# Performance work log

Measured on AMD Instinct MI355X. Metric: run time of the kernel, lower is better.

The kernel has to match this reference:

```python
import jax, jax.numpy as jnp
import numpy as np

D, L, W, K = 16, 1000000, 64, 8
PAD = (W - 1) // 2  # 31, matches padding1 in the torch code


def setup_inputs() -> dict:
    key = jax.random.key(0)
    kx, kp = jax.random.split(key)
    x = jax.random.normal(kx, (D, L), dtype=jnp.float32)
    # torch uses torch.rand (uniform [0,1)) for each of the K (D,W) parameters
    P = jax.random.uniform(kp, (K, D, W), dtype=jnp.float32)
    return {"x": x, "P": P}


def _fullscan(x, P):
    # x: (D, L); P: (K, D, W)
    p = PAD
    # --- middle positions k in [p, L-W+p]: standard valid correlation ---
    # mid[k_out, o] = sum_{d,m} x[d, o+m] * P[k_out, d, m], position k = o + p
    mid = jax.lax.conv_general_dilated(
        x[None],                      # (1, D, L)
        P,                            # (K, D, W)
        window_strides=(1,),
        padding="VALID",
        dimension_numbers=("NCH", "OIH", "NCH"),
    )[0]                              # (K, L-W+1)
    # --- left edge k in [0, p): data x[:, :k+W-p] * kernel[:, :k+W-p] ---
    # prefix[i, m] = sum_d x[d, m] * P[i, d, m] over the first W samples
    tl = jnp.einsum("dm,kdm->km", x[:, :W], P)        # (K, W)
    left_c = jnp.cumsum(tl, axis=1)                    # prefix sums
    left = left_c[:, W - p - 1 : W - 1]                # (K, p)
    # --- right edge k in (L-W+p, L): data x[:, k-p:] * kernel[:, W+k-L-p:] ---
    tr = jnp.einsum("dm,kdm->km", x[:, L - W :], P)    # (K, W)
    suf = jnp.cumsum(tr[:, ::-1], axis=1)[:, ::-1]     # suffix sums: suf[:, t] = sum_{m>=t}
    right = suf[:, 1 : W - p]                          # (K, W-1-p)
    y = jnp.concatenate([left, mid, right], axis=1)    # (K, L)
    return y.reshape(-1, 1)                            # (K*L, 1)


def reference(x, P):
    return _fullscan(x, P)
```

## Files before the change

### kernel.cpp

```cpp
#include <hip/hip_runtime.h>


constexpr int D    = 16;
constexpr int L    = 1000000;
constexpr int W    = 64;
constexpr int K    = 8;
constexpr int PADL = 31;
constexpr int NMID = L - W + 1;
constexpr int TPB  = 256;
constexpr int OTW  = 8;
constexpr int CTW  = OTW + 2;
constexpr int BLK_OUT = 4 * OTW * 32;
constexpr int XS   = 1104;
constexpr int NBLK = (NMID + BLK_OUT - 1) / BLK_OUT;
constexpr int NGRID = NBLK + K;

typedef __attribute__((ext_vector_type(8)))  short short8;
typedef __attribute__((ext_vector_type(16))) float floatx16;

__device__ __forceinline__ unsigned short f2bf(float f) {
    union { float f; unsigned u; } v; v.f = f;
    unsigned u = v.u + 0x7fff + ((v.u >> 16) & 1);
    return (unsigned short)(u >> 16);
}

__global__ __launch_bounds__(TPB, 3) void fullscan_mid(
    const float* __restrict__ x, const float* __restrict__ P,
    const unsigned short* __restrict__ afr, float* __restrict__ out)
{
    __shared__ __align__(16) unsigned short xs[XS * 16];
    const int bid = blockIdx.x;
    const int tid = threadIdx.x;

    if (bid >= NBLK) {
        const int k = bid - NBLK;
        const int j = tid;
        if (j < PADL) {
            float acc = 0.0f;
            for (int m = 0; m <= 32 + j; ++m)
#pragma unroll
                for (int d = 0; d < D; ++d)
                    acc = fmaf(x[d * L + m], P[(k * D + d) * W + m], acc);
            out[k * L + j] = acc;
        } else if (j < 2 * PADL + 1) {
            const int jj = j - PADL;
            float acc = 0.0f;
            for (int m = jj + 1; m < W; ++m)
#pragma unroll
                for (int d = 0; d < D; ++d)
                    acc = fmaf(x[d * L + (L - W) + m], P[(k * D + d) * W + m], acc);
            out[k * L + PADL + NMID + jj] = acc;
        }
        return;
    }

    const int s0   = bid * BLK_OUT;
    const int lane = tid & 63;
    const int wv   = tid >> 6;

    short8 A[16];
#pragma unroll
    for (int c = 0; c < 16; ++c)
        A[c] = *(const short8*)(afr + (c * 64 + lane) * 8);

    {
        const int pl = tid & 63;
        const int dq = tid >> 6;
        const float* xr0 = x + (4 * dq + 0) * L + s0;
        const float* xr1 = x + (4 * dq + 1) * L + s0;
        const float* xr2 = x + (4 * dq + 2) * L + s0;
        const float* xr3 = x + (4 * dq + 3) * L + s0;
#pragma unroll 1
        for (int b = 0; b < XS; b += 64) {
            const int pos = b + pl;
            if (pos < XS) {
                const bool ok = (s0 + pos) < L;
                const float v0 = ok ? xr0[pos] : 0.0f;
                const float v1 = ok ? xr1[pos] : 0.0f;
                const float v2 = ok ? xr2[pos] : 0.0f;
                const float v3 = ok ? xr3[pos] : 0.0f;
                unsigned long long w =
                    (unsigned long long)f2bf(v0)
                  | ((unsigned long long)f2bf(v1) << 16)
                  | ((unsigned long long)f2bf(v2) << 32)
                  | ((unsigned long long)f2bf(v3) << 48);
                const int swz = (pos >> 2) & 1;
                *(unsigned long long*)&xs[pos * 16 + ((dq * 4) ^ (swz * 8))] = w;
            }
        }
    }
    __syncthreads();

    const int n  = lane & 31;
    const int h  = lane >> 5;
    const int hb = h * 8;
    const int wbase = wv * OTW;

    floatx16 accW[3];

#pragma unroll
    for (int jj = 0; jj < CTW; ++jj) {
        floatx16 acc;
#pragma unroll
        for (int r = 0; r < 16; ++r) acc[r] = 0.0f;
        const int p0 = (wbase + jj) * 32 + n;

        short8 Bc = *(const short8*)
            &xs[p0 * 16 + (hb ^ (((p0 >> 2) & 1) * 8))];
#pragma unroll
        for (int c = 0; c < 16; ++c) {
            short8 Bn = Bc;
            if (c < 15) {
                const int pos = p0 + c + 1;
                Bn = *(const short8*)
                    &xs[pos * 16 + (hb ^ (((pos >> 2) & 1) * 8))];
            }
            acc = __builtin_amdgcn_mfma_f32_32x32x16_bf16(A[c], Bc, acc, 0, 0, 0);
            Bc = Bn;
        }
        accW[jj % 3] = acc;

        if (jj >= 2) {
            const int ot = jj - 2;
            const floatx16 a0 = accW[(jj - 2) % 3];
            const floatx16 a1 = accW[(jj - 1) % 3];
            const floatx16 a2 = accW[jj % 3];
            const int t = s0 + (wbase + ot) * 32 + n;
#pragma unroll
            for (int kk = 0; kk < 4; ++kk) {
                const float g1t = (n >= 16) ? a0[kk + 4]  : a1[kk + 4];
                const float g3t = (n >= 16) ? a1[kk + 12] : a2[kk + 12];
                const float v = a0[kk] + a1[kk + 8]
                              + __shfl_xor(g1t, 16, 64)
                              + __shfl_xor(g3t, 16, 64);
                if (t < NMID)
                    out[(kk + 4 * h) * L + PADL + t] = v;
            }
        }
    }
}

__global__ void fullscan_prep(const float* __restrict__ P,
                              unsigned short* __restrict__ afr)
{
    const int u = blockIdx.x * 256 + threadIdx.x;
    const int c = u >> 9, lane = (u >> 3) & 63, j = u & 7;
    const int m = lane & 31, h = lane >> 5;
    const int k = m & 7, g = m >> 3;
    const int d = 8 * h + j;
    const int w = 16 * g + c;
    afr[u] = f2bf(P[(k * D + d) * W + w]);
}

extern "C" void kernel_launch(void* const* d_in, const int* in_sizes, int n_in,
                              void* d_out, int out_size, void* d_ws, size_t ws_size,
                              hipStream_t stream)
{
    const float* x = (const float*)d_in[0];
    const float* P = (const float*)d_in[1];
    float* out = (float*)d_out;
    unsigned short* afr = (unsigned short*)d_ws;

    hipLaunchKernelGGL(fullscan_prep, dim3(32), dim3(256), 0, stream, P, afr);
    hipLaunchKernelGGL(fullscan_mid, dim3(NGRID), dim3(TPB), 0, stream,
                       x, P, afr, out);
}
```

Measured before the change: 139.1 us.

## Batch staging loads for more memory parallelism and move edge work to prep kernel

```diff
diff --git a/kernel.cpp b/kernel.cpp
--- a/kernel.cpp
+++ b/kernel.cpp
@@ -13,7 +13,6 @@
 constexpr int BLK_OUT = 4 * OTW * 32;
 constexpr int XS   = 1104;
 constexpr int NBLK = (NMID + BLK_OUT - 1) / BLK_OUT;
-constexpr int NGRID = NBLK + K;
 
 typedef __attribute__((ext_vector_type(8)))  short short8;
 typedef __attribute__((ext_vector_type(16))) float floatx16;
@@ -25,43 +24,14 @@
 }
 
 __global__ __launch_bounds__(TPB, 3) void fullscan_mid(
-    const float* __restrict__ x, const float* __restrict__ P,
+    const float* __restrict__ x,
     const unsigned short* __restrict__ afr, float* __restrict__ out)
 {
     __shared__ __align__(16) unsigned short xs[XS * 16];
-    const int bid = blockIdx.x;
     const int tid = threadIdx.x;
-
-    if (bid >= NBLK) {
-        const int k = bid - NBLK;
-        const int j = tid;
-        if (j < PADL) {
-            float acc = 0.0f;
-            for (int m = 0; m <= 32 + j; ++m)
-#pragma unroll
-                for (int d = 0; d < D; ++d)
-                    acc = fmaf(x[d * L + m], P[(k * D + d) * W + m], acc);
-            out[k * L + j] = acc;
-        } else if (j < 2 * PADL + 1) {
-            const int jj = j - PADL;
-            float acc = 0.0f;
-            for (int m = jj + 1; m < W; ++m)
-#pragma unroll
-                for (int d = 0; d < D; ++d)
-                    acc = fmaf(x[d * L + (L - W) + m], P[(k * D + d) * W + m], acc);
-            out[k * L + PADL + NMID + jj] = acc;
-        }
-        return;
-    }
-
-    const int s0   = bid * BLK_OUT;
+    const int s0  = blockIdx.x * BLK_OUT;
     const int lane = tid & 63;
     const int wv   = tid >> 6;
-
-    short8 A[16];
-#pragma unroll
-    for (int c = 0; c < 16; ++c)
-        A[c] = *(const short8*)(afr + (c * 64 + lane) * 8);
 
     {
         const int pl = tid & 63;
@@ -71,24 +41,38 @@
         const float* xr2 = x + (4 * dq + 2) * L + s0;
         const float* xr3 = x + (4 * dq + 3) * L + s0;
 #pragma unroll 1
-        for (int b = 0; b < XS; b += 64) {
-            const int pos = b + pl;
-            if (pos < XS) {
-                const bool ok = (s0 + pos) < L;
-                const float v0 = ok ? xr0[pos] : 0.0f;
-                const float v1 = ok ? xr1[pos] : 0.0f;
-                const float v2 = ok ? xr2[pos] : 0.0f;
-                const float v3 = ok ? xr3[pos] : 0.0f;
-                unsigned long long w =
-                    (unsigned long long)f2bf(v0)
-                  | ((unsigned long long)f2bf(v1) << 16)
-                  | ((unsigned long long)f2bf(v2) << 32)
-                  | ((unsigned long long)f2bf(v3) << 48);
-                const int swz = (pos >> 2) & 1;
-                *(unsigned long long*)&xs[pos * 16 + ((dq * 4) ^ (swz * 8))] = w;
+        for (int b0 = 0; b0 < XS; b0 += 256) {
+            float v[4][4];
+#pragma unroll
+            for (int s = 0; s < 4; ++s) {
+                const int pos = b0 + 64 * s + pl;
+                const bool ok = (pos < XS) && (s0 + pos < L);
+                v[s][0] = ok ? xr0[pos] : 0.0f;
+                v[s][1] = ok ? xr1[pos] : 0.0f;
+                v[s][2] = ok ? xr2[pos] : 0.0f;
+                v[s][3] = ok ? xr3[pos] : 0.0f;
+            }
+#pragma unroll
+            for (int s = 0; s < 4; ++s) {
+                const int pos = b0 + 64 * s + pl;
+                if (pos < XS) {
+                    unsigned long long w =
+                        (unsigned long long)f2bf(v[s][0])
+                      | ((unsigned long long)f2bf(v[s][1]) << 16)
+                      | ((unsigned long long)f2bf(v[s][2]) << 32)
+                      | ((unsigned long long)f2bf(v[s][3]) << 48);
+                    const int swz = (pos >> 2) & 1;
+                    *(unsigned long long*)&xs[pos * 16 + ((dq * 4) ^ (swz * 8))] = w;
+                }
             }
         }
     }
+
+    short8 A[16];
+#pragma unroll
+    for (int c = 0; c < 16; ++c)
+        A[c] = *(const short8*)(afr + (c * 64 + lane) * 8);
+
     __syncthreads();
 
     const int n  = lane & 31;
@@ -140,16 +124,39 @@
     }
 }
 
-__global__ void fullscan_prep(const float* __restrict__ P,
-                              unsigned short* __restrict__ afr)
+__global__ void fullscan_prep(
+    const float* __restrict__ x, const float* __restrict__ P,
+    unsigned short* __restrict__ afr, float* __restrict__ out)
 {
-    const int u = blockIdx.x * 256 + threadIdx.x;
-    const int c = u >> 9, lane = (u >> 3) & 63, j = u & 7;
-    const int m = lane & 31, h = lane >> 5;
-    const int k = m & 7, g = m >> 3;
-    const int d = 8 * h + j;
-    const int w = 16 * g + c;
-    afr[u] = f2bf(P[(k * D + d) * W + w]);
+    const int bid = blockIdx.x;
+    if (bid < 32) {
+        const int u = bid * 256 + threadIdx.x;
+        const int c = u >> 9, lane = (u >> 3) & 63, j = u & 7;
+        const int m = lane & 31, h = lane >> 5;
+        const int k = m & 7, g = m >> 3;
+        const int d = 8 * h + j;
+        const int w = 16 * g + c;
+        afr[u] = f2bf(P[(k * D + d) * W + w]);
+        return;
+    }
+    const int k = bid - 32;
+    const int j = threadIdx.x;
+    if (j < PADL) {
+        float acc = 0.0f;
+        for (int m = 0; m <= 32 + j; ++m)
+#pragma unroll
+            for (int d = 0; d < D; ++d)
+                acc = fmaf(x[d * L + m], P[(k * D + d) * W + m], acc);
+        out[k * L + j] = acc;
+    } else if (j < 2 * PADL + 1) {
+        const int jj = j - PADL;
+        float acc = 0.0f;
+        for (int m = jj + 1; m < W; ++m)
+#pragma unroll
+            for (int d = 0; d < D; ++d)
+                acc = fmaf(x[d * L + (L - W) + m], P[(k * D + d) * W + m], acc);
+        out[k * L + PADL + NMID + jj] = acc;
+    }
 }
 
 extern "C" void kernel_launch(void* const* d_in, const int* in_sizes, int n_in,
@@ -161,7 +168,8 @@
     float* out = (float*)d_out;
     unsigned short* afr = (unsigned short*)d_ws;
 
-    hipLaunchKernelGGL(fullscan_prep, dim3(32), dim3(256), 0, stream, P, afr);
-    hipLaunchKernelGGL(fullscan_mid, dim3(NGRID), dim3(TPB), 0, stream,
+    hipLaunchKernelGGL(fullscan_prep, dim3(40), dim3(256), 0, stream,
                        x, P, afr, out);
+    hipLaunchKernelGGL(fullscan_mid, dim3(NBLK), dim3(TPB), 0, stream,
+                       x, afr, out);
 }
```

Result: slower. 155.1 us (+11.5%).
